# Optimization experiments

Measured on AMD Instinct MI355X. Metric: run time of the kernel, lower is better.

## Reference

```python
import jax, jax.numpy as jnp
import numpy as np

B, V, C, D = 32, 64, 32, 256
VOCAB = 20000
NUM_T = 1000


def _run_lstm(x, Wih, Whh, b):
    # x: [T, B, H_in]; torch-style single-layer LSTM with zero initial state
    T, Bb, _ = x.shape
    H = Whh.shape[1]
    def step(carry, xt):
        h, c = carry
        z = xt @ Wih.T + h @ Whh.T + b
        i, f, g, o = jnp.split(z, 4, axis=-1)
        c = jax.nn.sigmoid(f) * c + jax.nn.sigmoid(i) * jnp.tanh(g)
        h = jax.nn.sigmoid(o) * jnp.tanh(c)
        return (h, c), h
    h0 = jnp.zeros((Bb, H), x.dtype)
    _, ys = jax.lax.scan(step, (h0, h0), x)
    return ys


def _forward(input_seqs, masks, lengths, seq_time_step, code_masks, emb, WQ1, WK1,
             decay, initial, lstm_Wih, lstm_Whh, lstm_b, hs_Wih, hs_Whh, hs_b,
             whk_W, whk_b, w1_W, w1_b, w2_W, w2_b, fuse_W, fuse_b, lab_W, lab_b,
             betas, Wdiff, diffusion_time_t, normal_noise):
    Bb, Vv, Cc = input_seqs.shape
    tok = input_seqs.reshape(-1, Cc)                      # [B*V, C]
    x = emb[tok]                                          # [B*V, C, D]
    q = x @ WQ1.T
    k = x @ WK1.T
    dp = jnp.einsum('bcd,bed->bce', q, k)                 # [B*V, C, C]
    cm = code_masks.reshape(-1, Cc)
    dp = dp - cm[:, None, :] - cm[:, :, None]
    sp = jax.nn.softmax(dp / jnp.sqrt(jnp.float32(D)), axis=-1)
    femb = jnp.einsum('bce,bed->bcd', sp, x)              # attended code embeddings
    femb = ((cm - 1e20) / -1e20)[:, :, None] * femb       # zero out padded codes
    dec = decay[tok][..., None]                           # [B*V, C, 1]
    ini = initial[tok][..., None]
    t = seq_time_step.reshape(-1)[:, None, None]          # [B*V, 1, 1]
    gate = jax.nn.sigmoid(dec * t + ini)                  # time-decay gate
    vv = jnp.einsum('bcx,bcd->bd', gate, femb)            # [B*V, D] visit vector
    vv = vv.reshape(Bb, Vv, -1).transpose(1, 0, 2)        # [V, B, D]

    lstm_out = _run_lstm(vv, lstm_Wih, lstm_Whh, lstm_b)  # [V, B, D]
    t_lstm = lstm_out.transpose(1, 0, 2)                  # [B, V, D]
    hiddenstate = _run_lstm(lstm_out, hs_Wih, hs_Whh, hs_b).transpose(1, 0, 2)

    # Vectorized form of the original per-step python loop.
    # NOTE: the original always uses e_k = t_lstm_out[:, 0:1, :] (step 0) -- kept faithfully.
    e_k = t_lstm[:, 0:1, :]                               # [B, 1, D]
    whp = hiddenstate[:, :-1, :] @ whk_W.T + whk_b        # [B, V-1, D]
    cat = jnp.concatenate([jnp.broadcast_to(e_k, whp.shape), whp], axis=-1)
    attn = jax.nn.softmax(jnp.tanh(cat @ w1_W.T + w1_b) @ w2_W.T + w2_b, axis=-1)
    rest = e_k * attn[..., 0:1] + whp * attn[..., 1:2]
    aligned = jnp.concatenate([e_k, rest], axis=1)        # [B, V, D]

    alpha = jnp.cumprod(1.0 - betas)[diffusion_time_t][:, None, None]
    noisy = aligned * jnp.sqrt(alpha) + normal_noise * jnp.sqrt(1.0 - alpha)
    predicted_noise = noisy @ Wdiff                       # surrogate for UNetModel (source not provided)
    gen = aligned + (normal_noise - predicted_noise)

    fused = jnp.concatenate([t_lstm, gen], axis=-1) @ fuse_W.T + fuse_b   # [B, V, D]
    mask_final = (jnp.arange(Vv)[None, :] == (lengths - 1)[:, None]).astype(fused.dtype)
    final = (fused * mask_final[:, :, None]).sum(axis=1)  # select last valid visit
    return final @ lab_W.T + lab_b                        # [B, 2]


def setup_inputs() -> dict:
    key = jax.random.key(0)
    ks = jax.random.split(key, 20)
    s = 0.05
    n = lambda i, shp: jax.random.normal(ks[i], shp, jnp.float32) * s
    emb = jax.random.normal(ks[0], (VOCAB + 1, D), jnp.float32) * 0.02
    emb = emb.at[VOCAB].set(0.0)  # padding_idx row
    return {
        'input_seqs': jax.random.randint(ks[1], (B, V, C), 0, VOCAB),
        'masks': jnp.zeros((B, V), jnp.float32),
        'lengths': jax.random.randint(ks[2], (B,), 1, V + 1),
        'seq_time_step': jax.random.uniform(ks[3], (B, V), jnp.float32),
        'code_masks': jnp.zeros((B, V, C), jnp.float32),
        'emb': emb,
        'WQ1': n(4, (D, D)), 'WK1': n(5, (D, D)),
        'decay': jnp.full((VOCAB + 1,), -0.1, jnp.float32),
        'initial': jnp.full((VOCAB + 1,), 1.0, jnp.float32),
        'lstm_Wih': n(6, (4 * D, D)), 'lstm_Whh': n(7, (4 * D, D)),
        'lstm_b': jnp.zeros((4 * D,), jnp.float32),
        'hs_Wih': n(8, (4 * D, D)), 'hs_Whh': n(9, (4 * D, D)),
        'hs_b': jnp.zeros((4 * D,), jnp.float32),
        'whk_W': n(10, (D, D)), 'whk_b': jnp.zeros((D,), jnp.float32),
        'w1_W': n(11, (64, 2 * D)), 'w1_b': jnp.zeros((64,), jnp.float32),
        'w2_W': n(12, (2, 64)), 'w2_b': jnp.zeros((2,), jnp.float32),
        'fuse_W': n(13, (D, 2 * D)), 'fuse_b': jnp.zeros((D,), jnp.float32),
        'lab_W': n(14, (2, D)), 'lab_b': jnp.zeros((2,), jnp.float32),
        'betas': jnp.linspace(1e-4, 0.02, NUM_T, dtype=jnp.float32),
        'Wdiff': n(15, (D, D)),
        'diffusion_time_t': jax.random.randint(ks[16], (B,), 0, NUM_T),
        'normal_noise': jax.random.normal(ks[17], (B, V, D), jnp.float32),
    }


def reference(input_seqs, masks, lengths, seq_time_step, code_masks, emb, WQ1, WK1,
              decay, initial, lstm_Wih, lstm_Whh, lstm_b, hs_Wih, hs_Whh, hs_b,
              whk_W, whk_b, w1_W, w1_b, w2_W, w2_b, fuse_W, fuse_b, lab_W, lab_b,
              betas, Wdiff, diffusion_time_t, normal_noise):
    return _forward(input_seqs, masks, lengths, seq_time_step, code_masks, emb, WQ1, WK1,
                    decay, initial, lstm_Wih, lstm_Whh, lstm_b, hs_Wih, hs_Whh, hs_b,
                    whk_W, whk_b, w1_W, w1_b, w2_W, w2_b, fuse_W, fuse_b, lab_W, lab_b,
                    betas, Wdiff, diffusion_time_t, normal_noise)
```

## Files before the change

### kernel.cpp

```cpp
#include <hip/hip_runtime.h>
#include <hip/hip_bf16.h>
#include <cmath>

typedef __attribute__((ext_vector_type(8))) short bf16x8;
typedef __attribute__((ext_vector_type(4))) float f32x4;
typedef __attribute__((ext_vector_type(4))) int i32x4;
typedef __attribute__((ext_vector_type(2))) unsigned int u32x2;

__device__ __forceinline__ float bf2f(unsigned short u) {
    unsigned int x = ((unsigned int)u) << 16;
    return __builtin_bit_cast(float, x);
}
__device__ __forceinline__ unsigned short f2bf(float f) {
    unsigned int x = __builtin_bit_cast(unsigned int, f);
    unsigned int lsb = (x >> 16) & 1u;
    x += 0x7fffu + lsb;
    return (unsigned short)(x >> 16);
}
__device__ __forceinline__ float sigm(float z) {
    return 1.f / (1.f + __expf(-z));
}
__device__ __forceinline__ float rcpf(float x) { return __builtin_amdgcn_rcpf(x); }
__device__ __forceinline__ float sigm_f(float z) { return rcpf(1.f + __expf(-z)); }
__device__ __forceinline__ float tanh_f(float z) { return 1.f - 2.f * rcpf(1.f + __expf(2.f * z)); }

__device__ __forceinline__ long ldg_sc8l(const void* p) {
    long r;
    asm volatile("global_load_dwordx2 %0, %1, off sc1" : "=v"(r) : "v"(p) : "memory");
    return r;
}
__device__ __forceinline__ u32x2 ldg_sc_u2(const void* p) {
    u32x2 r;
    asm volatile("global_load_dwordx2 %0, %1, off sc1" : "=v"(r) : "v"(p) : "memory");
    return r;
}
__device__ __forceinline__ void stg_sc_u2(void* p, u32x2 v) {
    asm volatile("global_store_dwordx2 %0, %1, off sc1" :: "v"(p), "v"(v) : "memory");
}
__device__ __forceinline__ void stg_sc_b(void* p, int v) {
    asm volatile("global_store_byte %0, %1, off sc1" :: "v"(p), "v"(v) : "memory");
}

__global__ void __launch_bounds__(256) pack_all(
    const float* __restrict__ Whh1, const float* __restrict__ Wih2,
    const float* __restrict__ Whh2, const float* __restrict__ Wih1,
    const float* __restrict__ WQ1, const float* __restrict__ WK1,
    const float* __restrict__ betas, const int* __restrict__ dift,
    const float* __restrict__ whk_W, const float* __restrict__ fuse_W,
    const float* __restrict__ w1_W,
    long* __restrict__ Wq, float* __restrict__ cs,
    unsigned short* __restrict__ W1h, unsigned short* __restrict__ M_pk,
    float* __restrict__ alpha, int* __restrict__ flags,
    float* __restrict__ whkT, float* __restrict__ fuseT,
    float* __restrict__ w1T) {
    int blk = blockIdx.x, tid = threadIdx.x;
    if (blk < 384) {
        int R = blk * 8 + (tid >> 5);
        int mat = R >> 10;
        int n = R & 1023;
        int t32 = tid & 31;
        const float* src = (mat == 0) ? Whh1 : (mat == 1 ? Wih2 : Whh2);
        const float* rp = src + (size_t)n * 256 + t32 * 8;
        float v[8];
        float mx = 0.f;
        for (int j = 0; j < 8; ++j) { v[j] = rp[j]; mx = fmaxf(mx, fabsf(v[j])); }
        for (int m = 1; m <= 16; m <<= 1) mx = fmaxf(mx, __shfl_xor(mx, m));
        float inv = mx > 0.f ? 127.f / mx : 0.f;
        unsigned int lo = 0, hi = 0;
        for (int j = 0; j < 4; ++j) {
            int iv = __float2int_rn(v[j] * inv);
            lo |= ((unsigned int)(unsigned char)(signed char)iv) << (8 * j);
            int iv2 = __float2int_rn(v[4 + j] * inv);
            hi |= ((unsigned int)(unsigned char)(signed char)iv2) << (8 * j);
        }
        int g = n >> 8, rem = n & 255;
        int w8 = rem >> 5, dt = (rem >> 4) & 1, cc = rem & 15;
        int t8 = g * 2 + dt;
        int kb = t32 >> 2, q = t32 & 3;
        unsigned int* dst = (unsigned int*)Wq +
            ((size_t)((mat * 512 + w8 * 64 + t8 * 8 + kb) * 64) + q * 16 + cc) * 2;
        dst[0] = lo;
        dst[1] = hi;
        if (t32 == 0) cs[mat * 1024 + n] = mx / 16129.f;
    } else if (blk < 512) {
        int cch = (blk - 384) * 256 + tid;
        int nt = cch >> 9;
        int r = cch & 511;
        int kb = r >> 6;
        int lane = r & 63;
        int grow = nt * 16 + (lane & 15);
        int k0 = kb * 32 + (lane >> 4) * 8;
        const float* sp = Wih1 + (size_t)grow * 256 + k0;
        bf16x8 hi;
        for (int j = 0; j < 8; ++j) hi[j] = (short)f2bf(sp[j]);
        *reinterpret_cast<bf16x8*>(W1h + (size_t)cch * 8) = hi;
    } else if (blk == 512) {
        if (tid < 32) {
            int tb = dift[tid];
            float p = 1.f;
            for (int i = 0; i <= tb; ++i) p *= (1.f - betas[i]);
            alpha[tid] = p;
        }
    } else if (blk == 513) {
        for (int i = tid; i < 2048; i += 256) flags[i] = 0;
    } else if (blk < 578) {
        int gid = (blk - 514) * 256 + tid;
        for (int i = 0; i < 4; ++i) {
            int e = gid + i * 16384;
            int k = e >> 8, dd = e & 255;
            whkT[e] = whk_W[(size_t)dd * 256 + k];
        }
    } else if (blk < 706) {
        int gid = (blk - 578) * 256 + tid;
        for (int i = 0; i < 4; ++i) {
            int e = gid + i * 32768;
            int k = e >> 8, dd = e & 255;
            fuseT[e] = fuse_W[(size_t)dd * 512 + k];
        }
    } else if (blk < 738) {
        int gid = (blk - 706) * 256 + tid;
        for (int i = 0; i < 4; ++i) {
            int e = gid + i * 8192;
            int k = e >> 6, j = e & 63;
            w1T[e] = w1_W[(size_t)j * 512 + k];
        }
    } else {
        __shared__ unsigned short As[256][32];
        __shared__ unsigned short Bs[256][32];
        int bx = blk - 738;
        int e0 = (bx >> 3) << 5;
        int f0 = (bx & 7) << 5;
        int col = tid & 31, rr = tid >> 5;
        for (int rep = 0; rep < 32; ++rep) {
            int d = rep * 8 + rr;
            As[d][col] = f2bf(WQ1[d * 256 + e0 + col]);
            Bs[d][col] = f2bf(WK1[d * 256 + f0 + col]);
        }
        __syncthreads();
        int el = tid & 31;
        int fl0 = tid >> 5;
        for (int i = 0; i < 4; ++i) {
            int fl = fl0 + 8 * i;
            float acc = 0.f;
            for (int d = 0; d < 256; ++d)
                acc += bf2f(As[d][el]) * bf2f(Bs[d][fl]);
            int e = e0 + el, f = f0 + fl;
            int kb = e >> 5, r = (e >> 3) & 3, j = e & 7;
            int nb = f >> 4;
            int lane = (r << 4) | (f & 15);
            M_pk[(((nb * 8 + kb) * 64) + lane) * 8 + j] = f2bf(acc);
        }
    }
}

__global__ void __launch_bounds__(256) attn_bags(
    const int* __restrict__ seqs, const float* __restrict__ tstep,
    const float* __restrict__ cmask, const float* __restrict__ emb,
    const float* __restrict__ decay, const float* __restrict__ initial,
    const unsigned short* __restrict__ M_pk, float* __restrict__ vv) {
    __shared__ __align__(16) unsigned short x_bf[32 * 256];
    __shared__ __align__(16) unsigned short t1_bf[32 * 256];
    __shared__ float dp_f[32 * 33];
    __shared__ float gate_sh[32];
    __shared__ float cm_sh[32];
    __shared__ int tok_sh[32];
    __shared__ float w_sh[32];

    int bag = blockIdx.x;
    int tid = threadIdx.x;

    if (tid < 32) {
        int tok = seqs[bag * 32 + tid];
        tok_sh[tid] = tok;
        float cm = cmask[bag * 32 + tid];
        cm_sh[tid] = cm;
        float tt = tstep[bag];
        float g = sigm(decay[tok] * tt + initial[tok]);
        g *= (cm - 1e20f) / (-1e20f);
        gate_sh[tid] = g;
    }
    __syncthreads();

    for (int it = 0; it < 8; ++it) {
        int fidx = it * 256 + tid;
        int c = fidx >> 6;
        int f4 = fidx & 63;
        const float4* src = reinterpret_cast<const float4*>(emb + (size_t)tok_sh[c] * 256) + f4;
        float4 vx = *src;
        int colx = f4 * 4;
        int eidx = c * 256 + (colx ^ ((c & 7) << 3));
        ushort4 w;
        w.x = f2bf(vx.x); w.y = f2bf(vx.y); w.z = f2bf(vx.z); w.w = f2bf(vx.w);
        *reinterpret_cast<ushort4*>(&x_bf[eidx]) = w;
    }
    __syncthreads();

    int wv = tid >> 6;
    int lane = tid & 63;
    int lr = lane & 15;
    int lk = lane >> 4;

    f32x4 acc[2][4];
    for (int a = 0; a < 2; ++a)
        for (int n = 0; n < 4; ++n) acc[a][n] = (f32x4){0.f, 0.f, 0.f, 0.f};
    for (int kb = 0; kb < 8; ++kb) {
        bf16x8 afr[2];
        for (int mb = 0; mb < 2; ++mb) {
            int row = mb * 16 + lr;
            int colx = kb * 32 + lk * 8;
            afr[mb] = *reinterpret_cast<const bf16x8*>(&x_bf[row * 256 + (colx ^ ((row & 7) << 3))]);
        }
        for (int nbi = 0; nbi < 4; ++nbi) {
            int nb = wv * 4 + nbi;
            bf16x8 bfr = *reinterpret_cast<const bf16x8*>(M_pk + (((nb * 8 + kb) * 64) + lane) * 8);
            acc[0][nbi] = __builtin_amdgcn_mfma_f32_16x16x32_bf16(afr[0], bfr, acc[0][nbi], 0, 0, 0);
            acc[1][nbi] = __builtin_amdgcn_mfma_f32_16x16x32_bf16(afr[1], bfr, acc[1][nbi], 0, 0, 0);
        }
    }
    for (int mb = 0; mb < 2; ++mb)
        for (int nbi = 0; nbi < 4; ++nbi)
            for (int r = 0; r < 4; ++r) {
                int row = mb * 16 + lk * 4 + r;
                int colx = wv * 64 + nbi * 16 + lr;
                t1_bf[row * 256 + (colx ^ ((row & 7) << 3))] = f2bf(acc[mb][nbi][r]);
            }
    __syncthreads();

    {
        int mb = wv >> 1, nb2 = wv & 1;
        f32x4 dacc = (f32x4){0.f, 0.f, 0.f, 0.f};
        for (int kb = 0; kb < 8; ++kb) {
            int cola = kb * 32 + lk * 8;
            int rowa = mb * 16 + lr;
            bf16x8 afr = *reinterpret_cast<const bf16x8*>(&t1_bf[rowa * 256 + (cola ^ ((rowa & 7) << 3))]);
            int rowb = nb2 * 16 + lr;
            bf16x8 bfr = *reinterpret_cast<const bf16x8*>(&x_bf[rowb * 256 + (cola ^ ((rowb & 7) << 3))]);
            dacc = __builtin_amdgcn_mfma_f32_16x16x32_bf16(afr, bfr, dacc, 0, 0, 0);
        }
        for (int r = 0; r < 4; ++r) {
            int c = mb * 16 + lk * 4 + r;
            int e = nb2 * 16 + lr;
            dp_f[c * 33 + e] = dacc[r];
        }
    }
    __syncthreads();

    if (tid < 32) {
        int c = tid;
        float cmc = cm_sh[c];
        float lg[32];
        float mx = -1e30f;
        for (int e = 0; e < 32; ++e) {
            float l = (dp_f[c * 33 + e] - cmc - cm_sh[e]) * 0.0625f;
            lg[e] = l;
            mx = fmaxf(mx, l);
        }
        float s = 0.f;
        for (int e = 0; e < 32; ++e) { float ex = __expf(lg[e] - mx); lg[e] = ex; s += ex; }
        float inv = 1.f / s;
        for (int e = 0; e < 32; ++e) dp_f[c * 33 + e] = lg[e] * inv;
    }
    __syncthreads();
    if (tid < 32) {
        int e = tid;
        float a2 = 0.f;
        for (int c = 0; c < 32; ++c) a2 += gate_sh[c] * dp_f[c * 33 + e];
        w_sh[e] = a2;
    }
    __syncthreads();

    float accv = 0.f;
    int d = tid;
    for (int e = 0; e < 32; ++e)
        accv += w_sh[e] * bf2f(x_bf[e * 256 + (d ^ ((e & 7) << 3))]);
    vv[(size_t)bag * 256 + d] = accv;
}

__global__ void __launch_bounds__(256) x1_mfma(const float* __restrict__ vv,
                                               const unsigned short* __restrict__ W1h,
                                               const float* __restrict__ lstm_b,
                                               unsigned short* __restrict__ X1bf) {
    __shared__ __align__(16) unsigned short xs[32 * 256];
    int blk = blockIdx.x;
    int rb = blk >> 3, gb = blk & 7;
    int tid = threadIdx.x;
    for (int it = 0; it < 8; ++it) {
        int idx = it * 256 + tid;
        int row = idx >> 6, f4 = idx & 63;
        float4 v = *reinterpret_cast<const float4*>(vv + (size_t)(rb * 32 + row) * 256 + f4 * 4);
        ushort4 w;
        w.x = f2bf(v.x); w.y = f2bf(v.y); w.z = f2bf(v.z); w.w = f2bf(v.w);
        *reinterpret_cast<ushort4*>(&xs[row * 256 + ((f4 * 4) ^ ((row & 7) << 3))]) = w;
    }
    __syncthreads();
    int wv = tid >> 6, lane = tid & 63, cl = lane & 15, kh = lane >> 4;
    f32x4 acc[2][2];
    for (int n = 0; n < 2; ++n) {
        int nt = gb * 8 + wv * 2 + n;
        float bz = lstm_b[nt * 16 + cl];
        acc[n][0] = (f32x4){bz, bz, bz, bz};
        acc[n][1] = (f32x4){bz, bz, bz, bz};
    }
    #pragma unroll
    for (int kb = 0; kb < 8; ++kb) {
        int k = kb * 32 + kh * 8;
        bf16x8 a0 = *reinterpret_cast<const bf16x8*>(&xs[cl * 256 + (k ^ ((cl & 7) << 3))]);
        bf16x8 a1 = *reinterpret_cast<const bf16x8*>(&xs[(16 + cl) * 256 + (k ^ (((16 + cl) & 7) << 3))]);
        for (int n = 0; n < 2; ++n) {
            int nt = gb * 8 + wv * 2 + n;
            size_t o = ((size_t)(nt * 8 + kb) * 64 + lane) * 8;
            bf16x8 bh = *reinterpret_cast<const bf16x8*>(W1h + o);
            acc[n][0] = __builtin_amdgcn_mfma_f32_16x16x32_bf16(a0, bh, acc[n][0], 0, 0, 0);
            acc[n][1] = __builtin_amdgcn_mfma_f32_16x16x32_bf16(a1, bh, acc[n][1], 0, 0, 0);
        }
    }
    for (int n = 0; n < 2; ++n) {
        int nt = gb * 8 + wv * 2 + n;
        int g = nt * 16 + cl;
        int dX = g & 255, gt = g >> 8;
        for (int mt = 0; mt < 2; ++mt)
            for (int r = 0; r < 4; ++r) {
                int row = rb * 32 + mt * 16 + kh * 4 + r;
                int b = row >> 6, t = row & 63;
                X1bf[((size_t)t * 32 + b) * 1024 + dX * 4 + gt] = f2bf(acc[n][mt][r]);
            }
    }
}

__global__ void __launch_bounds__(512, 2) lstm_persist(
    const long* __restrict__ Wq, const float* __restrict__ cs,
    const unsigned short* __restrict__ X1bf, const float* __restrict__ hs_b,
    unsigned short* __restrict__ h1bf, unsigned short* __restrict__ h2bf,
    signed char* h1q, unsigned short* p1, int* flags) {
    int role = blockIdx.x;
    int half = role & 1;
    int kind = role >> 1;
    int tid = threadIdx.x;
    int w = tid >> 6, lane = tid & 63, c = lane & 15, q = lane >> 4;

    long wt[64];
    #pragma unroll
    for (int t8 = 0; t8 < 8; ++t8)
        #pragma unroll
        for (int kb = 0; kb < 8; ++kb)
            wt[t8 * 8 + kb] = Wq[(size_t)((kind * 512 + w * 64 + t8 * 8 + kb) * 64) + lane];
    float csv[8];
    #pragma unroll
    for (int t8 = 0; t8 < 8; ++t8) {
        int g = t8 >> 1, dt = t8 & 1;
        csv[t8] = cs[kind * 1024 + g * 256 + w * 32 + dt * 16 + c];
    }

    if (kind == 0) {
        __shared__ signed char hq[2][16][272];
        float cstate[8] = {0.f, 0.f, 0.f, 0.f, 0.f, 0.f, 0.f, 0.f};
        int B0 = half * 16 + q * 4;
        int dbase = w * 32;
        for (int t = 0; t < 64; ++t) {
            ushort4 xv[8];
            #pragma unroll
            for (int dt = 0; dt < 2; ++dt)
                #pragma unroll
                for (int r = 0; r < 4; ++r) {
                    int B = B0 + r, d = dbase + dt * 16 + c;
                    xv[dt * 4 + r] = *reinterpret_cast<const ushort4*>(
                        X1bf + ((size_t)(t * 32 + B) * 1024 + d * 4));
                }
            i32x4 acc[8];
            #pragma unroll
            for (int i = 0; i < 8; ++i) acc[i] = (i32x4){0, 0, 0, 0};
            if (t > 0) {
                int pb = (t - 1) & 1;
                long a[8];
                #pragma unroll
                for (int kb = 0; kb < 8; ++kb)
                    a[kb] = *reinterpret_cast<const long*>(&hq[pb][c][kb * 32 + q * 8]);
                #pragma unroll
                for (int t8 = 0; t8 < 8; ++t8)
                    #pragma unroll
                    for (int kb = 0; kb < 8; ++kb)
                        acc[t8] = __builtin_amdgcn_mfma_i32_16x16x32_i8(
                            a[kb], wt[t8 * 8 + kb], acc[t8], 0, 0, 0);
            }
            #pragma unroll
            for (int dt = 0; dt < 2; ++dt)
                #pragma unroll
                for (int r = 0; r < 4; ++r) {
                    int idx = dt * 4 + r;
                    ushort4 x = xv[idx];
                    float zi = (float)acc[0 + dt][r] * csv[0 + dt] + bf2f(x.x);
                    float zf = (float)acc[2 + dt][r] * csv[2 + dt] + bf2f(x.y);
                    float zg = (float)acc[4 + dt][r] * csv[4 + dt] + bf2f(x.z);
                    float zo = (float)acc[6 + dt][r] * csv[6 + dt] + bf2f(x.w);
                    float cn = sigm_f(zf) * cstate[idx] + sigm_f(zi) * tanh_f(zg);
                    float hn = sigm_f(zo) * tanh_f(cn);
                    cstate[idx] = cn;
                    int B = B0 + r, d = dbase + dt * 16 + c;
                    h1bf[(size_t)(t * 32 + B) * 256 + d] = f2bf(hn);
                    int hv = __float2int_rn(hn * 127.f);
                    hq[t & 1][q * 4 + r][d] = (signed char)hv;
                    stg_sc_b(h1q + (size_t)(t * 32 + B) * 256 + d, hv);
                }
            asm volatile("s_waitcnt vmcnt(0)" ::: "memory");
            if (lane == 0)
                __hip_atomic_store(flags + t * 16 + half * 8 + w, 1,
                                   __ATOMIC_RELAXED, __HIP_MEMORY_SCOPE_AGENT);
            __syncthreads();
        }
    } else if (kind == 1) {
        for (int s = 0; s < 64; ++s) {
            const int* f = flags + s * 16 + half * 8;
            while (1) {
                int v = 1;
                if (lane < 8)
                    v = __hip_atomic_load(f + lane, __ATOMIC_RELAXED, __HIP_MEMORY_SCOPE_AGENT);
                if (__all(v != 0)) break;
                __builtin_amdgcn_s_sleep(1);
            }
            __builtin_amdgcn_sched_barrier(0);
            const signed char* hb = h1q + (size_t)(s * 32 + half * 16) * 256;
            long a[8];
            #pragma unroll
            for (int kb = 0; kb < 8; ++kb)
                a[kb] = ldg_sc8l(hb + c * 256 + kb * 32 + q * 8);
            asm volatile("s_waitcnt vmcnt(0)" ::: "memory");
            __builtin_amdgcn_sched_barrier(0);
            i32x4 acc[8];
            #pragma unroll
            for (int i = 0; i < 8; ++i) acc[i] = (i32x4){0, 0, 0, 0};
            #pragma unroll
            for (int t8 = 0; t8 < 8; ++t8)
                #pragma unroll
                for (int kb = 0; kb < 8; ++kb)
                    acc[t8] = __builtin_amdgcn_mfma_i32_16x16x32_i8(
                        a[kb], wt[t8 * 8 + kb], acc[t8], 0, 0, 0);
            #pragma unroll
            for (int t8 = 0; t8 < 8; ++t8) {
                int g = t8 >> 1, dt = t8 & 1;
                int n = g * 256 + w * 32 + dt * 16 + c;
                u32x2 pv;
                pv.x = (unsigned int)f2bf((float)acc[t8][0] * csv[t8]) |
                       ((unsigned int)f2bf((float)acc[t8][1] * csv[t8]) << 16);
                pv.y = (unsigned int)f2bf((float)acc[t8][2] * csv[t8]) |
                       ((unsigned int)f2bf((float)acc[t8][3] * csv[t8]) << 16);
                stg_sc_u2(p1 + ((size_t)(s * 2 + half) * 1024 + n) * 16 + q * 4, pv);
            }
            asm volatile("s_waitcnt vmcnt(0)" ::: "memory");
            if (lane == 0)
                __hip_atomic_store(flags + 1024 + s * 16 + half * 8 + w, 1,
                                   __ATOMIC_RELAXED, __HIP_MEMORY_SCOPE_AGENT);
        }
    } else {
        __shared__ signed char hq2[2][16][272];
        float cstate[8] = {0.f, 0.f, 0.f, 0.f, 0.f, 0.f, 0.f, 0.f};
        float bias[8];
        #pragma unroll
        for (int t8 = 0; t8 < 8; ++t8) {
            int g = t8 >> 1, dt = t8 & 1;
            bias[t8] = hs_b[g * 256 + w * 32 + dt * 16 + c];
        }
        int B0 = half * 16 + q * 4;
        int dbase = w * 32;
        for (int s = 0; s < 64; ++s) {
            const int* fp = flags + 1024 + s * 16 + half * 8 + w;
            while (__hip_atomic_load(fp, __ATOMIC_RELAXED, __HIP_MEMORY_SCOPE_AGENT) == 0)
                __builtin_amdgcn_s_sleep(1);
            __builtin_amdgcn_sched_barrier(0);
            u32x2 pv[8];
            #pragma unroll
            for (int t8 = 0; t8 < 8; ++t8) {
                int g = t8 >> 1, dt = t8 & 1;
                int n = g * 256 + w * 32 + dt * 16 + c;
                pv[t8] = ldg_sc_u2(p1 + ((size_t)(s * 2 + half) * 1024 + n) * 16 + q * 4);
            }
            i32x4 acc[8];
            #pragma unroll
            for (int i = 0; i < 8; ++i) acc[i] = (i32x4){0, 0, 0, 0};
            if (s > 0) {
                int pb = (s - 1) & 1;
                long a[8];
                #pragma unroll
                for (int kb = 0; kb < 8; ++kb)
                    a[kb] = *reinterpret_cast<const long*>(&hq2[pb][c][kb * 32 + q * 8]);
                asm volatile("s_waitcnt vmcnt(0)" ::: "memory");
                __builtin_amdgcn_sched_barrier(0);
                #pragma unroll
                for (int t8 = 0; t8 < 8; ++t8)
                    #pragma unroll
                    for (int kb = 0; kb < 8; ++kb)
                        acc[t8] = __builtin_amdgcn_mfma_i32_16x16x32_i8(
                            a[kb], wt[t8 * 8 + kb], acc[t8], 0, 0, 0);
            } else {
                asm volatile("s_waitcnt vmcnt(0)" ::: "memory");
                __builtin_amdgcn_sched_barrier(0);
            }
            #pragma unroll
            for (int dt = 0; dt < 2; ++dt)
                #pragma unroll
                for (int r = 0; r < 4; ++r) {
                    int idx = dt * 4 + r;
                    float p_i = bf2f((unsigned short)((r < 2 ? pv[0 + dt].x : pv[0 + dt].y) >> ((r & 1) * 16)));
                    float p_f = bf2f((unsigned short)((r < 2 ? pv[2 + dt].x : pv[2 + dt].y) >> ((r & 1) * 16)));
                    float p_g = bf2f((unsigned short)((r < 2 ? pv[4 + dt].x : pv[4 + dt].y) >> ((r & 1) * 16)));
                    float p_o = bf2f((unsigned short)((r < 2 ? pv[6 + dt].x : pv[6 + dt].y) >> ((r & 1) * 16)));
                    float zi = (float)acc[0 + dt][r] * csv[0 + dt] + p_i + bias[0 + dt];
                    float zf = (float)acc[2 + dt][r] * csv[2 + dt] + p_f + bias[2 + dt];
                    float zg = (float)acc[4 + dt][r] * csv[4 + dt] + p_g + bias[4 + dt];
                    float zo = (float)acc[6 + dt][r] * csv[6 + dt] + p_o + bias[6 + dt];
                    float cn = sigm_f(zf) * cstate[idx] + sigm_f(zi) * tanh_f(zg);
                    float hn = sigm_f(zo) * tanh_f(cn);
                    cstate[idx] = cn;
                    int B = B0 + r, d = dbase + dt * 16 + c;
                    h2bf[(size_t)(s * 32 + B) * 256 + d] = f2bf(hn);
                    hq2[s & 1][q * 4 + r][d] = (signed char)__float2int_rn(hn * 127.f);
                }
            __syncthreads();
        }
    }
}

__global__ void __launch_bounds__(256) tail_k(
    const int* __restrict__ lengths,
    const unsigned short* __restrict__ h1, const unsigned short* __restrict__ h2,
    const float* __restrict__ whkT, const float* __restrict__ whk_b,
    const float* __restrict__ w1T, const float* __restrict__ w1_b,
    const float* __restrict__ w2_W, const float* __restrict__ w2_b,
    const float* __restrict__ fuseT, const float* __restrict__ fuse_b,
    const float* __restrict__ lab_W, const float* __restrict__ lab_b,
    const float* __restrict__ Wdiff, const float* __restrict__ alpha,
    const float* __restrict__ noise, float* __restrict__ out) {
    __shared__ float ek[256], tv[256], hs[256], whp[256], a1s[64];
    __shared__ float noisy_s[256], fin[512], fused_s[256], attn_s[2];
    int b = blockIdx.x, tid = threadIdx.x;
    int vstar = lengths[b] - 1;
    {
        ek[tid] = bf2f(h1[(size_t)b * 256 + tid]);
        tv[tid] = bf2f(h1[((size_t)vstar * 32 + b) * 256 + tid]);
        if (vstar > 0)
            hs[tid] = bf2f(h2[((size_t)(vstar - 1) * 32 + b) * 256 + tid]);
    }
    __syncthreads();

    float aligned;
    if (vstar > 0) {
        float s0 = 0.f, s1 = 0.f, s2 = 0.f, s3 = 0.f;
        for (int k = 0; k < 256; k += 4) {
            s0 += whkT[(k + 0) * 256 + tid] * hs[k + 0];
            s1 += whkT[(k + 1) * 256 + tid] * hs[k + 1];
            s2 += whkT[(k + 2) * 256 + tid] * hs[k + 2];
            s3 += whkT[(k + 3) * 256 + tid] * hs[k + 3];
        }
        whp[tid] = whk_b[tid] + s0 + s1 + s2 + s3;
        __syncthreads();
        if (tid < 64) {
            float a0 = 0.f, a1 = 0.f, a2 = 0.f, a3 = 0.f;
            for (int k = 0; k < 256; k += 4) {
                a0 += w1T[(k + 0) * 64 + tid] * ek[k + 0];
                a1 += w1T[(k + 1) * 64 + tid] * ek[k + 1];
                a2 += w1T[(k + 2) * 64 + tid] * ek[k + 2];
                a3 += w1T[(k + 3) * 64 + tid] * ek[k + 3];
            }
            for (int k = 0; k < 256; k += 4) {
                a0 += w1T[(256 + k + 0) * 64 + tid] * whp[k + 0];
                a1 += w1T[(256 + k + 1) * 64 + tid] * whp[k + 1];
                a2 += w1T[(256 + k + 2) * 64 + tid] * whp[k + 2];
                a3 += w1T[(256 + k + 3) * 64 + tid] * whp[k + 3];
            }
            a1s[tid] = tanhf(w1_b[tid] + a0 + a1 + a2 + a3);
        }
        __syncthreads();
        if (tid < 2) {
            float a3 = w2_b[tid];
            const float* wr2 = w2_W + tid * 64;
            for (int k = 0; k < 64; ++k) a3 += wr2[k] * a1s[k];
            attn_s[tid] = a3;
        }
        __syncthreads();
        float m = fmaxf(attn_s[0], attn_s[1]);
        float e0 = __expf(attn_s[0] - m), e1 = __expf(attn_s[1] - m);
        float inv = 1.f / (e0 + e1);
        aligned = ek[tid] * (e0 * inv) + whp[tid] * (e1 * inv);
    } else {
        aligned = ek[tid];
    }

    float al = alpha[b];
    float sa = sqrtf(al), sb = sqrtf(1.f - al);
    float nz = noise[((size_t)b * 64 + vstar) * 256 + tid];
    noisy_s[tid] = aligned * sa + nz * sb;
    __syncthreads();
    {
        float p0 = 0.f, p1v = 0.f, p2 = 0.f, p3 = 0.f;
        for (int k = 0; k < 256; k += 4) {
            p0 += noisy_s[k + 0] * Wdiff[(size_t)(k + 0) * 256 + tid];
            p1v += noisy_s[k + 1] * Wdiff[(size_t)(k + 1) * 256 + tid];
            p2 += noisy_s[k + 2] * Wdiff[(size_t)(k + 2) * 256 + tid];
            p3 += noisy_s[k + 3] * Wdiff[(size_t)(k + 3) * 256 + tid];
        }
        float gen = aligned + nz - (p0 + p1v + p2 + p3);
        fin[tid] = tv[tid];
        fin[256 + tid] = gen;
    }
    __syncthreads();
    {
        float f0 = 0.f, f1 = 0.f, f2 = 0.f, f3 = 0.f;
        for (int k = 0; k < 512; k += 4) {
            f0 += fuseT[(k + 0) * 256 + tid] * fin[k + 0];
            f1 += fuseT[(k + 1) * 256 + tid] * fin[k + 1];
            f2 += fuseT[(k + 2) * 256 + tid] * fin[k + 2];
            f3 += fuseT[(k + 3) * 256 + tid] * fin[k + 3];
        }
        fused_s[tid] = fuse_b[tid] + f0 + f1 + f2 + f3;
    }
    __syncthreads();
    if (tid < 2) {
        float o = lab_b[tid];
        const float* lw = lab_W + tid * 256;
        for (int k = 0; k < 256; ++k) o += lw[k] * fused_s[k];
        out[b * 2 + tid] = o;
    }
}

extern "C" void kernel_launch(void* const* d_in, const int* in_sizes, int n_in,
                              void* d_out, int out_size, void* d_ws, size_t ws_size,
                              hipStream_t stream) {
    const int*   seqs    = (const int*)  d_in[0];
    const int*   lengths = (const int*)  d_in[2];
    const float* tstep   = (const float*)d_in[3];
    const float* cmask   = (const float*)d_in[4];
    const float* emb     = (const float*)d_in[5];
    const float* WQ1     = (const float*)d_in[6];
    const float* WK1     = (const float*)d_in[7];
    const float* decay   = (const float*)d_in[8];
    const float* initial = (const float*)d_in[9];
    const float* Wih1    = (const float*)d_in[10];
    const float* Whh1    = (const float*)d_in[11];
    const float* lstm_b  = (const float*)d_in[12];
    const float* Wih2    = (const float*)d_in[13];
    const float* Whh2    = (const float*)d_in[14];
    const float* hs_b    = (const float*)d_in[15];
    const float* whk_W   = (const float*)d_in[16];
    const float* whk_b   = (const float*)d_in[17];
    const float* w1_W    = (const float*)d_in[18];
    const float* w1_b    = (const float*)d_in[19];
    const float* w2_W    = (const float*)d_in[20];
    const float* w2_b    = (const float*)d_in[21];
    const float* fuse_W  = (const float*)d_in[22];
    const float* fuse_b  = (const float*)d_in[23];
    const float* lab_W   = (const float*)d_in[24];
    const float* lab_b   = (const float*)d_in[25];
    const float* betas   = (const float*)d_in[26];
    const float* Wdiff   = (const float*)d_in[27];
    const int*   dift    = (const int*)  d_in[28];
    const float* noise   = (const float*)d_in[29];
    float* out = (float*)d_out;

    float* ws = (float*)d_ws;
    size_t off = 0;
    auto alloc = [&](size_t nfloats) { size_t r = off; off += (nfloats + 63) & ~(size_t)63; return r; };
    unsigned short* M_pk  = (unsigned short*)(ws + alloc(32768));
    float*          alpha = ws + alloc(64);
    float*          cs    = ws + alloc(3072);
    int*            flags = (int*)(ws + alloc(2048));
    float*          vv    = ws + alloc(524288);
    unsigned short* X1bf  = (unsigned short*)(ws + alloc(1048576));
    unsigned short* h1bf  = (unsigned short*)(ws + alloc(262144));
    unsigned short* h2bf  = (unsigned short*)(ws + alloc(262144));
    unsigned short* p1    = (unsigned short*)(ws + alloc(1048576));
    long*           Wq    = (long*)(ws + alloc(196608));
    unsigned short* W1h   = (unsigned short*)(ws + alloc(131072));
    float*          whkT  = ws + alloc(65536);
    float*          fuseT = ws + alloc(131072);
    float*          w1T   = ws + alloc(32768);
    signed char*    h1q   = (signed char*)vv;

    pack_all<<<802, 256, 0, stream>>>(Whh1, Wih2, Whh2, Wih1, WQ1, WK1, betas, dift,
                                      whk_W, fuse_W, w1_W,
                                      Wq, cs, W1h, M_pk, alpha, flags,
                                      whkT, fuseT, w1T);
    attn_bags<<<2048, 256, 0, stream>>>(seqs, tstep, cmask, emb, decay, initial, M_pk, vv);
    x1_mfma<<<512, 256, 0, stream>>>(vv, W1h, lstm_b, X1bf);
    lstm_persist<<<6, 512, 0, stream>>>(Wq, cs, X1bf, hs_b, h1bf, h2bf, h1q, p1, flags);
    tail_k<<<32, 256, 0, stream>>>(lengths, h1bf, h2bf, whkT, whk_b,
                                   w1T, w1_b, w2_W, w2_b, fuseT, fuse_b,
                                   lab_W, lab_b, Wdiff, alpha, noise, out);
}
```

Before: 340.9 us.

## Fuse attention, input projection and LSTM into one kernel with counter-based dataflow

Merges the attention-bag, input-projection and persistent LSTM kernels into a single launch. The 6 LSTM role blocks come first, followed by attention blocks and then projection blocks. Global atomic counters gate each stage, so the LSTM can start on early timesteps while later visit vectors and projections are still being computed. This removes launch boundaries and overlaps the serial recurrence with the parallel front end. The cost is spin-wait polling and a dependence on the persistent blocks being co-resident, plus a separate h1q buffer and 512-thread blocks for the attention work.

```diff
diff --git a/kernel.cpp b/kernel.cpp
--- a/kernel.cpp
+++ b/kernel.cpp
@@ -34,11 +34,23 @@
     asm volatile("global_load_dwordx2 %0, %1, off sc1" : "=v"(r) : "v"(p) : "memory");
     return r;
 }
+__device__ __forceinline__ f32x4 ldg_sc16(const void* p) {
+    f32x4 r;
+    asm volatile("global_load_dwordx4 %0, %1, off sc1" : "=v"(r) : "v"(p) : "memory");
+    return r;
+}
 __device__ __forceinline__ void stg_sc_u2(void* p, u32x2 v) {
     asm volatile("global_store_dwordx2 %0, %1, off sc1" :: "v"(p), "v"(v) : "memory");
 }
 __device__ __forceinline__ void stg_sc_b(void* p, int v) {
     asm volatile("global_store_byte %0, %1, off sc1" :: "v"(p), "v"(v) : "memory");
+}
+__device__ __forceinline__ void stg_sc_dw(void* p, float v) {
+    asm volatile("global_store_dword %0, %1, off sc1" :: "v"(p), "v"(v) : "memory");
+}
+__device__ __forceinline__ void stg_sc_sh(void* p, unsigned short v) {
+    unsigned int vx = v;
+    asm volatile("global_store_short %0, %1, off sc1" :: "v"(p), "v"(vx) : "memory");
 }
 
 __global__ void __launch_bounds__(256) pack_all(
@@ -102,7 +114,7 @@
             alpha[tid] = p;
         }
     } else if (blk == 513) {
-        for (int i = tid; i < 2048; i += 256) flags[i] = 0;
+        for (int i = tid; i < 4096; i += 256) flags[i] = 0;
     } else if (blk < 578) {
         int gid = (blk - 514) * 256 + tid;
         for (int i = 0; i < 4; ++i) {
@@ -153,369 +165,407 @@
     }
 }
 
-__global__ void __launch_bounds__(256) attn_bags(
+__global__ void __launch_bounds__(512, 2) fused_main(
     const int* __restrict__ seqs, const float* __restrict__ tstep,
     const float* __restrict__ cmask, const float* __restrict__ emb,
     const float* __restrict__ decay, const float* __restrict__ initial,
-    const unsigned short* __restrict__ M_pk, float* __restrict__ vv) {
-    __shared__ __align__(16) unsigned short x_bf[32 * 256];
-    __shared__ __align__(16) unsigned short t1_bf[32 * 256];
-    __shared__ float dp_f[32 * 33];
-    __shared__ float gate_sh[32];
-    __shared__ float cm_sh[32];
-    __shared__ int tok_sh[32];
-    __shared__ float w_sh[32];
-
-    int bag = blockIdx.x;
-    int tid = threadIdx.x;
-
-    if (tid < 32) {
-        int tok = seqs[bag * 32 + tid];
-        tok_sh[tid] = tok;
-        float cm = cmask[bag * 32 + tid];
-        cm_sh[tid] = cm;
-        float tt = tstep[bag];
-        float g = sigm(decay[tok] * tt + initial[tok]);
-        g *= (cm - 1e20f) / (-1e20f);
-        gate_sh[tid] = g;
-    }
-    __syncthreads();
-
-    for (int it = 0; it < 8; ++it) {
-        int fidx = it * 256 + tid;
-        int c = fidx >> 6;
-        int f4 = fidx & 63;
-        const float4* src = reinterpret_cast<const float4*>(emb + (size_t)tok_sh[c] * 256) + f4;
-        float4 vx = *src;
-        int colx = f4 * 4;
-        int eidx = c * 256 + (colx ^ ((c & 7) << 3));
-        ushort4 w;
-        w.x = f2bf(vx.x); w.y = f2bf(vx.y); w.z = f2bf(vx.z); w.w = f2bf(vx.w);
-        *reinterpret_cast<ushort4*>(&x_bf[eidx]) = w;
-    }
-    __syncthreads();
-
-    int wv = tid >> 6;
-    int lane = tid & 63;
-    int lr = lane & 15;
-    int lk = lane >> 4;
-
-    f32x4 acc[2][4];
-    for (int a = 0; a < 2; ++a)
-        for (int n = 0; n < 4; ++n) acc[a][n] = (f32x4){0.f, 0.f, 0.f, 0.f};
-    for (int kb = 0; kb < 8; ++kb) {
-        bf16x8 afr[2];
-        for (int mb = 0; mb < 2; ++mb) {
-            int row = mb * 16 + lr;
-            int colx = kb * 32 + lk * 8;
-            afr[mb] = *reinterpret_cast<const bf16x8*>(&x_bf[row * 256 + (colx ^ ((row & 7) << 3))]);
-        }
-        for (int nbi = 0; nbi < 4; ++nbi) {
-            int nb = wv * 4 + nbi;
-            bf16x8 bfr = *reinterpret_cast<const bf16x8*>(M_pk + (((nb * 8 + kb) * 64) + lane) * 8);
-            acc[0][nbi] = __builtin_amdgcn_mfma_f32_16x16x32_bf16(afr[0], bfr, acc[0][nbi], 0, 0, 0);
-            acc[1][nbi] = __builtin_amdgcn_mfma_f32_16x16x32_bf16(afr[1], bfr, acc[1][nbi], 0, 0, 0);
-        }
-    }
-    for (int mb = 0; mb < 2; ++mb)
-        for (int nbi = 0; nbi < 4; ++nbi)
-            for (int r = 0; r < 4; ++r) {
-                int row = mb * 16 + lk * 4 + r;
-                int colx = wv * 64 + nbi * 16 + lr;
-                t1_bf[row * 256 + (colx ^ ((row & 7) << 3))] = f2bf(acc[mb][nbi][r]);
-            }
-    __syncthreads();
-
-    {
-        int mb = wv >> 1, nb2 = wv & 1;
-        f32x4 dacc = (f32x4){0.f, 0.f, 0.f, 0.f};
-        for (int kb = 0; kb < 8; ++kb) {
-            int cola = kb * 32 + lk * 8;
-            int rowa = mb * 16 + lr;
-            bf16x8 afr = *reinterpret_cast<const bf16x8*>(&t1_bf[rowa * 256 + (cola ^ ((rowa & 7) << 3))]);
-            int rowb = nb2 * 16 + lr;
-            bf16x8 bfr = *reinterpret_cast<const bf16x8*>(&x_bf[rowb * 256 + (cola ^ ((rowb & 7) << 3))]);
-            dacc = __builtin_amdgcn_mfma_f32_16x16x32_bf16(afr, bfr, dacc, 0, 0, 0);
-        }
-        for (int r = 0; r < 4; ++r) {
-            int c = mb * 16 + lk * 4 + r;
-            int e = nb2 * 16 + lr;
-            dp_f[c * 33 + e] = dacc[r];
-        }
-    }
-    __syncthreads();
-
-    if (tid < 32) {
-        int c = tid;
-        float cmc = cm_sh[c];
-        float lg[32];
-        float mx = -1e30f;
-        for (int e = 0; e < 32; ++e) {
-            float l = (dp_f[c * 33 + e] - cmc - cm_sh[e]) * 0.0625f;
-            lg[e] = l;
-            mx = fmaxf(mx, l);
-        }
-        float s = 0.f;
-        for (int e = 0; e < 32; ++e) { float ex = __expf(lg[e] - mx); lg[e] = ex; s += ex; }
-        float inv = 1.f / s;
-        for (int e = 0; e < 32; ++e) dp_f[c * 33 + e] = lg[e] * inv;
-    }
-    __syncthreads();
-    if (tid < 32) {
-        int e = tid;
-        float a2 = 0.f;
-        for (int c = 0; c < 32; ++c) a2 += gate_sh[c] * dp_f[c * 33 + e];
-        w_sh[e] = a2;
-    }
-    __syncthreads();
-
-    float accv = 0.f;
-    int d = tid;
-    for (int e = 0; e < 32; ++e)
-        accv += w_sh[e] * bf2f(x_bf[e * 256 + (d ^ ((e & 7) << 3))]);
-    vv[(size_t)bag * 256 + d] = accv;
-}
-
-__global__ void __launch_bounds__(256) x1_mfma(const float* __restrict__ vv,
-                                               const unsigned short* __restrict__ W1h,
-                                               const float* __restrict__ lstm_b,
-                                               unsigned short* __restrict__ X1bf) {
-    __shared__ __align__(16) unsigned short xs[32 * 256];
-    int blk = blockIdx.x;
-    int rb = blk >> 3, gb = blk & 7;
-    int tid = threadIdx.x;
-    for (int it = 0; it < 8; ++it) {
-        int idx = it * 256 + tid;
-        int row = idx >> 6, f4 = idx & 63;
-        float4 v = *reinterpret_cast<const float4*>(vv + (size_t)(rb * 32 + row) * 256 + f4 * 4);
-        ushort4 w;
-        w.x = f2bf(v.x); w.y = f2bf(v.y); w.z = f2bf(v.z); w.w = f2bf(v.w);
-        *reinterpret_cast<ushort4*>(&xs[row * 256 + ((f4 * 4) ^ ((row & 7) << 3))]) = w;
-    }
-    __syncthreads();
-    int wv = tid >> 6, lane = tid & 63, cl = lane & 15, kh = lane >> 4;
-    f32x4 acc[2][2];
-    for (int n = 0; n < 2; ++n) {
-        int nt = gb * 8 + wv * 2 + n;
-        float bz = lstm_b[nt * 16 + cl];
-        acc[n][0] = (f32x4){bz, bz, bz, bz};
-        acc[n][1] = (f32x4){bz, bz, bz, bz};
-    }
-    #pragma unroll
-    for (int kb = 0; kb < 8; ++kb) {
-        int k = kb * 32 + kh * 8;
-        bf16x8 a0 = *reinterpret_cast<const bf16x8*>(&xs[cl * 256 + (k ^ ((cl & 7) << 3))]);
-        bf16x8 a1 = *reinterpret_cast<const bf16x8*>(&xs[(16 + cl) * 256 + (k ^ (((16 + cl) & 7) << 3))]);
-        for (int n = 0; n < 2; ++n) {
-            int nt = gb * 8 + wv * 2 + n;
-            size_t o = ((size_t)(nt * 8 + kb) * 64 + lane) * 8;
-            bf16x8 bh = *reinterpret_cast<const bf16x8*>(W1h + o);
-            acc[n][0] = __builtin_amdgcn_mfma_f32_16x16x32_bf16(a0, bh, acc[n][0], 0, 0, 0);
-            acc[n][1] = __builtin_amdgcn_mfma_f32_16x16x32_bf16(a1, bh, acc[n][1], 0, 0, 0);
-        }
-    }
-    for (int n = 0; n < 2; ++n) {
-        int nt = gb * 8 + wv * 2 + n;
-        int g = nt * 16 + cl;
-        int dX = g & 255, gt = g >> 8;
-        for (int mt = 0; mt < 2; ++mt)
-            for (int r = 0; r < 4; ++r) {
-                int row = rb * 32 + mt * 16 + kh * 4 + r;
-                int b = row >> 6, t = row & 63;
-                X1bf[((size_t)t * 32 + b) * 1024 + dX * 4 + gt] = f2bf(acc[n][mt][r]);
-            }
-    }
-}
-
-__global__ void __launch_bounds__(512, 2) lstm_persist(
+    const unsigned short* __restrict__ M_pk, float* __restrict__ vv,
+    const unsigned short* __restrict__ W1h, const float* __restrict__ lstm_b,
+    unsigned short* __restrict__ X1bf,
     const long* __restrict__ Wq, const float* __restrict__ cs,
-    const unsigned short* __restrict__ X1bf, const float* __restrict__ hs_b,
+    const float* __restrict__ hs_b,
     unsigned short* __restrict__ h1bf, unsigned short* __restrict__ h2bf,
     signed char* h1q, unsigned short* p1, int* flags) {
-    int role = blockIdx.x;
-    int half = role & 1;
-    int kind = role >> 1;
-    int tid = threadIdx.x;
-    int w = tid >> 6, lane = tid & 63, c = lane & 15, q = lane >> 4;
-
-    long wt[64];
-    #pragma unroll
-    for (int t8 = 0; t8 < 8; ++t8)
+    __shared__ __align__(16) unsigned char smem[37504];
+    int blk = blockIdx.x;
+    int* cnt_vv = flags + 2048;
+    int* cnt_x1 = flags + 2112;
+
+    if (blk < 6) {
+        int role = blk;
+        int half = role & 1;
+        int kind = role >> 1;
+        int tid = threadIdx.x;
+        int w = tid >> 6, lane = tid & 63, c = lane & 15, q = lane >> 4;
+
+        long wt[64];
         #pragma unroll
-        for (int kb = 0; kb < 8; ++kb)
-            wt[t8 * 8 + kb] = Wq[(size_t)((kind * 512 + w * 64 + t8 * 8 + kb) * 64) + lane];
-    float csv[8];
-    #pragma unroll
-    for (int t8 = 0; t8 < 8; ++t8) {
-        int g = t8 >> 1, dt = t8 & 1;
-        csv[t8] = cs[kind * 1024 + g * 256 + w * 32 + dt * 16 + c];
-    }
-
-    if (kind == 0) {
-        __shared__ signed char hq[2][16][272];
-        float cstate[8] = {0.f, 0.f, 0.f, 0.f, 0.f, 0.f, 0.f, 0.f};
-        int B0 = half * 16 + q * 4;
-        int dbase = w * 32;
-        for (int t = 0; t < 64; ++t) {
-            ushort4 xv[8];
+        for (int t8 = 0; t8 < 8; ++t8)
             #pragma unroll
-            for (int dt = 0; dt < 2; ++dt)
-                #pragma unroll
-                for (int r = 0; r < 4; ++r) {
-                    int B = B0 + r, d = dbase + dt * 16 + c;
-                    xv[dt * 4 + r] = *reinterpret_cast<const ushort4*>(
-                        X1bf + ((size_t)(t * 32 + B) * 1024 + d * 4));
+            for (int kb = 0; kb < 8; ++kb)
+                wt[t8 * 8 + kb] = Wq[(size_t)((kind * 512 + w * 64 + t8 * 8 + kb) * 64) + lane];
+        float csv[8];
+        #pragma unroll
+        for (int t8 = 0; t8 < 8; ++t8) {
+            int g = t8 >> 1, dt = t8 & 1;
+            csv[t8] = cs[kind * 1024 + g * 256 + w * 32 + dt * 16 + c];
+        }
+
+        if (kind == 0) {
+            auto hq = (signed char (*)[16][272])smem;
+            float cstate[8] = {0.f, 0.f, 0.f, 0.f, 0.f, 0.f, 0.f, 0.f};
+            int B0 = half * 16 + q * 4;
+            int dbase = w * 32;
+            for (int t = 0; t < 64; ++t) {
+                if ((t & 31) == 0) {
+                    const int* cp = cnt_x1 + half * 2 + (t >> 5);
+                    while (__hip_atomic_load(cp, __ATOMIC_RELAXED, __HIP_MEMORY_SCOPE_AGENT) < 128)
+                        __builtin_amdgcn_s_sleep(8);
+                    __builtin_amdgcn_sched_barrier(0);
                 }
-            i32x4 acc[8];
-            #pragma unroll
-            for (int i = 0; i < 8; ++i) acc[i] = (i32x4){0, 0, 0, 0};
-            if (t > 0) {
-                int pb = (t - 1) & 1;
+                u32x2 xq[8];
+                #pragma unroll
+                for (int dt = 0; dt < 2; ++dt)
+                    #pragma unroll
+                    for (int r = 0; r < 4; ++r) {
+                        int B = B0 + r, d = dbase + dt * 16 + c;
+                        xq[dt * 4 + r] = ldg_sc_u2(X1bf + ((size_t)(t * 32 + B) * 1024 + d * 4));
+                    }
+                i32x4 acc[8];
+                #pragma unroll
+                for (int i = 0; i < 8; ++i) acc[i] = (i32x4){0, 0, 0, 0};
+                if (t > 0) {
+                    int pb = (t - 1) & 1;
+                    long a[8];
+                    #pragma unroll
+                    for (int kb = 0; kb < 8; ++kb)
+                        a[kb] = *reinterpret_cast<const long*>(&hq[pb][c][kb * 32 + q * 8]);
+                    #pragma unroll
+                    for (int t8 = 0; t8 < 8; ++t8)
+                        #pragma unroll
+                        for (int kb = 0; kb < 8; ++kb)
+                            acc[t8] = __builtin_amdgcn_mfma_i32_16x16x32_i8(
+                                a[kb], wt[t8 * 8 + kb], acc[t8], 0, 0, 0);
+                }
+                asm volatile("s_waitcnt vmcnt(0)" ::: "memory");
+                __builtin_amdgcn_sched_barrier(0);
+                #pragma unroll
+                for (int dt = 0; dt < 2; ++dt)
+                    #pragma unroll
+                    for (int r = 0; r < 4; ++r) {
+                        int idx = dt * 4 + r;
+                        u32x2 x = xq[idx];
+                        float zi = (float)acc[0 + dt][r] * csv[0 + dt] + bf2f((unsigned short)(x.x & 0xFFFFu));
+                        float zf = (float)acc[2 + dt][r] * csv[2 + dt] + bf2f((unsigned short)(x.x >> 16));
+                        float zg = (float)acc[4 + dt][r] * csv[4 + dt] + bf2f((unsigned short)(x.y & 0xFFFFu));
+                        float zo = (float)acc[6 + dt][r] * csv[6 + dt] + bf2f((unsigned short)(x.y >> 16));
+                        float cn = sigm_f(zf) * cstate[idx] + sigm_f(zi) * tanh_f(zg);
+                        float hn = sigm_f(zo) * tanh_f(cn);
+                        cstate[idx] = cn;
+                        int B = B0 + r, d = dbase + dt * 16 + c;
+                        h1bf[(size_t)(t * 32 + B) * 256 + d] = f2bf(hn);
+                        int hv = __float2int_rn(hn * 127.f);
+                        hq[t & 1][q * 4 + r][d] = (signed char)hv;
+                        stg_sc_b(h1q + (size_t)(t * 32 + B) * 256 + d, hv);
+                    }
+                asm volatile("s_waitcnt vmcnt(0)" ::: "memory");
+                if (lane == 0)
+                    __hip_atomic_store(flags + t * 16 + half * 8 + w, 1,
+                                       __ATOMIC_RELAXED, __HIP_MEMORY_SCOPE_AGENT);
+                __syncthreads();
+            }
+        } else if (kind == 1) {
+            for (int s = 0; s < 64; ++s) {
+                const int* f = flags + s * 16 + half * 8;
+                while (1) {
+                    int v = 1;
+                    if (lane < 8)
+                        v = __hip_atomic_load(f + lane, __ATOMIC_RELAXED, __HIP_MEMORY_SCOPE_AGENT);
+                    if (__all(v != 0)) break;
+                    __builtin_amdgcn_s_sleep(1);
+                }
+                __builtin_amdgcn_sched_barrier(0);
+                const signed char* hb = h1q + (size_t)(s * 32 + half * 16) * 256;
                 long a[8];
                 #pragma unroll
                 for (int kb = 0; kb < 8; ++kb)
-                    a[kb] = *reinterpret_cast<const long*>(&hq[pb][c][kb * 32 + q * 8]);
+                    a[kb] = ldg_sc8l(hb + c * 256 + kb * 32 + q * 8);
+                asm volatile("s_waitcnt vmcnt(0)" ::: "memory");
+                __builtin_amdgcn_sched_barrier(0);
+                i32x4 acc[8];
+                #pragma unroll
+                for (int i = 0; i < 8; ++i) acc[i] = (i32x4){0, 0, 0, 0};
                 #pragma unroll
                 for (int t8 = 0; t8 < 8; ++t8)
                     #pragma unroll
                     for (int kb = 0; kb < 8; ++kb)
                         acc[t8] = __builtin_amdgcn_mfma_i32_16x16x32_i8(
                             a[kb], wt[t8 * 8 + kb], acc[t8], 0, 0, 0);
-            }
-            #pragma unroll
-            for (int dt = 0; dt < 2; ++dt)
-                #pragma unroll
-                for (int r = 0; r < 4; ++r) {
-                    int idx = dt * 4 + r;
-                    ushort4 x = xv[idx];
-                    float zi = (float)acc[0 + dt][r] * csv[0 + dt] + bf2f(x.x);
-                    float zf = (float)acc[2 + dt][r] * csv[2 + dt] + bf2f(x.y);
-                    float zg = (float)acc[4 + dt][r] * csv[4 + dt] + bf2f(x.z);
-                    float zo = (float)acc[6 + dt][r] * csv[6 + dt] + bf2f(x.w);
-                    float cn = sigm_f(zf) * cstate[idx] + sigm_f(zi) * tanh_f(zg);
-                    float hn = sigm_f(zo) * tanh_f(cn);
-                    cstate[idx] = cn;
-                    int B = B0 + r, d = dbase + dt * 16 + c;
-                    h1bf[(size_t)(t * 32 + B) * 256 + d] = f2bf(hn);
-                    int hv = __float2int_rn(hn * 127.f);
-                    hq[t & 1][q * 4 + r][d] = (signed char)hv;
-                    stg_sc_b(h1q + (size_t)(t * 32 + B) * 256 + d, hv);
+                #pragma unroll
+                for (int t8 = 0; t8 < 8; ++t8) {
+                    int g = t8 >> 1, dt = t8 & 1;
+                    int n = g * 256 + w * 32 + dt * 16 + c;
+                    u32x2 pv;
+                    pv.x = (unsigned int)f2bf((float)acc[t8][0] * csv[t8]) |
+                           ((unsigned int)f2bf((float)acc[t8][1] * csv[t8]) << 16);
+                    pv.y = (unsigned int)f2bf((float)acc[t8][2] * csv[t8]) |
+                           ((unsigned int)f2bf((float)acc[t8][3] * csv[t8]) << 16);
+                    stg_sc_u2(p1 + ((size_t)(s * 2 + half) * 1024 + n) * 16 + q * 4, pv);
                 }
-            asm volatile("s_waitcnt vmcnt(0)" ::: "memory");
-            if (lane == 0)
-                __hip_atomic_store(flags + t * 16 + half * 8 + w, 1,
-                                   __ATOMIC_RELAXED, __HIP_MEMORY_SCOPE_AGENT);
-            __syncthreads();
-        }
-    } else if (kind == 1) {
-        for (int s = 0; s < 64; ++s) {
-            const int* f = flags + s * 16 + half * 8;
-            while (1) {
-                int v = 1;
-                if (lane < 8)
-                    v = __hip_atomic_load(f + lane, __ATOMIC_RELAXED, __HIP_MEMORY_SCOPE_AGENT);
-                if (__all(v != 0)) break;
-                __builtin_amdgcn_s_sleep(1);
-            }
-            __builtin_amdgcn_sched_barrier(0);
-            const signed char* hb = h1q + (size_t)(s * 32 + half * 16) * 256;
-            long a[8];
-            #pragma unroll
-            for (int kb = 0; kb < 8; ++kb)
-                a[kb] = ldg_sc8l(hb + c * 256 + kb * 32 + q * 8);
-            asm volatile("s_waitcnt vmcnt(0)" ::: "memory");
-            __builtin_amdgcn_sched_barrier(0);
-            i32x4 acc[8];
-            #pragma unroll
-            for (int i = 0; i < 8; ++i) acc[i] = (i32x4){0, 0, 0, 0};
-            #pragma unroll
-            for (int t8 = 0; t8 < 8; ++t8)
-                #pragma unroll
-                for (int kb = 0; kb < 8; ++kb)
-                    acc[t8] = __builtin_amdgcn_mfma_i32_16x16x32_i8(
-                        a[kb], wt[t8 * 8 + kb], acc[t8], 0, 0, 0);
+                asm volatile("s_waitcnt vmcnt(0)" ::: "memory");
+                if (lane == 0)
+                    __hip_atomic_store(flags + 1024 + s * 16 + half * 8 + w, 1,
+                                       __ATOMIC_RELAXED, __HIP_MEMORY_SCOPE_AGENT);
+            }
+        } else {
+            auto hq2 = (signed char (*)[16][272])smem;
+            float cstate[8] = {0.f, 0.f, 0.f, 0.f, 0.f, 0.f, 0.f, 0.f};
+            float bias[8];
             #pragma unroll
             for (int t8 = 0; t8 < 8; ++t8) {
                 int g = t8 >> 1, dt = t8 & 1;
-                int n = g * 256 + w * 32 + dt * 16 + c;
-                u32x2 pv;
-                pv.x = (unsigned int)f2bf((float)acc[t8][0] * csv[t8]) |
-                       ((unsigned int)f2bf((float)acc[t8][1] * csv[t8]) << 16);
-                pv.y = (unsigned int)f2bf((float)acc[t8][2] * csv[t8]) |
-                       ((unsigned int)f2bf((float)acc[t8][3] * csv[t8]) << 16);
-                stg_sc_u2(p1 + ((size_t)(s * 2 + half) * 1024 + n) * 16 + q * 4, pv);
-            }
-            asm volatile("s_waitcnt vmcnt(0)" ::: "memory");
-            if (lane == 0)
-                __hip_atomic_store(flags + 1024 + s * 16 + half * 8 + w, 1,
-                                   __ATOMIC_RELAXED, __HIP_MEMORY_SCOPE_AGENT);
-        }
-    } else {
-        __shared__ signed char hq2[2][16][272];
-        float cstate[8] = {0.f, 0.f, 0.f, 0.f, 0.f, 0.f, 0.f, 0.f};
-        float bias[8];
-        #pragma unroll
-        for (int t8 = 0; t8 < 8; ++t8) {
-            int g = t8 >> 1, dt = t8 & 1;
-            bias[t8] = hs_b[g * 256 + w * 32 + dt * 16 + c];
-        }
-        int B0 = half * 16 + q * 4;
-        int dbase = w * 32;
-        for (int s = 0; s < 64; ++s) {
-            const int* fp = flags + 1024 + s * 16 + half * 8 + w;
-            while (__hip_atomic_load(fp, __ATOMIC_RELAXED, __HIP_MEMORY_SCOPE_AGENT) == 0)
-                __builtin_amdgcn_s_sleep(1);
-            __builtin_amdgcn_sched_barrier(0);
-            u32x2 pv[8];
-            #pragma unroll
-            for (int t8 = 0; t8 < 8; ++t8) {
-                int g = t8 >> 1, dt = t8 & 1;
-                int n = g * 256 + w * 32 + dt * 16 + c;
-                pv[t8] = ldg_sc_u2(p1 + ((size_t)(s * 2 + half) * 1024 + n) * 16 + q * 4);
-            }
-            i32x4 acc[8];
-            #pragma unroll
-            for (int i = 0; i < 8; ++i) acc[i] = (i32x4){0, 0, 0, 0};
-            if (s > 0) {
-                int pb = (s - 1) & 1;
-                long a[8];
-                #pragma unroll
-                for (int kb = 0; kb < 8; ++kb)
-                    a[kb] = *reinterpret_cast<const long*>(&hq2[pb][c][kb * 32 + q * 8]);
-                asm volatile("s_waitcnt vmcnt(0)" ::: "memory");
+                bias[t8] = hs_b[g * 256 + w * 32 + dt * 16 + c];
+            }
+            int B0 = half * 16 + q * 4;
+            int dbase = w * 32;
+            for (int s = 0; s < 64; ++s) {
+                const int* fp = flags + 1024 + s * 16 + half * 8 + w;
+                while (__hip_atomic_load(fp, __ATOMIC_RELAXED, __HIP_MEMORY_SCOPE_AGENT) == 0)
+                    __builtin_amdgcn_s_sleep(1);
                 __builtin_amdgcn_sched_barrier(0);
-                #pragma unroll
-                for (int t8 = 0; t8 < 8; ++t8)
+                u32x2 pv[8];
+                #pragma unroll
+                for (int t8 = 0; t8 < 8; ++t8) {
+                    int g = t8 >> 1, dt = t8 & 1;
+                    int n = g * 256 + w * 32 + dt * 16 + c;
+                    pv[t8] = ldg_sc_u2(p1 + ((size_t)(s * 2 + half) * 1024 + n) * 16 + q * 4);
+                }
+                i32x4 acc[8];
+                #pragma unroll
+                for (int i = 0; i < 8; ++i) acc[i] = (i32x4){0, 0, 0, 0};
+                if (s > 0) {
+                    int pb = (s - 1) & 1;
+                    long a[8];
                     #pragma unroll
                     for (int kb = 0; kb < 8; ++kb)
-                        acc[t8] = __builtin_amdgcn_mfma_i32_16x16x32_i8(
-                            a[kb], wt[t8 * 8 + kb], acc[t8], 0, 0, 0);
-            } else {
-                asm volatile("s_waitcnt vmcnt(0)" ::: "memory");
-                __builtin_amdgcn_sched_barrier(0);
-            }
-            #pragma unroll
-            for (int dt = 0; dt < 2; ++dt)
-                #pragma unroll
+                        a[kb] = *reinterpret_cast<const long*>(&hq2[pb][c][kb * 32 + q * 8]);
+                    asm volatile("s_waitcnt vmcnt(0)" ::: "memory");
+                    __builtin_amdgcn_sched_barrier(0);
+                    #pragma unroll
+                    for (int t8 = 0; t8 < 8; ++t8)
+                        #pragma unroll
+                        for (int kb = 0; kb < 8; ++kb)
+                            acc[t8] = __builtin_amdgcn_mfma_i32_16x16x32_i8(
+                                a[kb], wt[t8 * 8 + kb], acc[t8], 0, 0, 0);
+                } else {
+                    asm volatile("s_waitcnt vmcnt(0)" ::: "memory");
+                    __builtin_amdgcn_sched_barrier(0);
+                }
+                #pragma unroll
+                for (int dt = 0; dt < 2; ++dt)
+                    #pragma unroll
+                    for (int r = 0; r < 4; ++r) {
+                        int idx = dt * 4 + r;
+                        float p_i = bf2f((unsigned short)((r < 2 ? pv[0 + dt].x : pv[0 + dt].y) >> ((r & 1) * 16)));
+                        float p_f = bf2f((unsigned short)((r < 2 ? pv[2 + dt].x : pv[2 + dt].y) >> ((r & 1) * 16)));
+                        float p_g = bf2f((unsigned short)((r < 2 ? pv[4 + dt].x : pv[4 + dt].y) >> ((r & 1) * 16)));
+                        float p_o = bf2f((unsigned short)((r < 2 ? pv[6 + dt].x : pv[6 + dt].y) >> ((r & 1) * 16)));
+                        float zi = (float)acc[0 + dt][r] * csv[0 + dt] + p_i + bias[0 + dt];
+                        float zf = (float)acc[2 + dt][r] * csv[2 + dt] + p_f + bias[2 + dt];
+                        float zg = (float)acc[4 + dt][r] * csv[4 + dt] + p_g + bias[4 + dt];
+                        float zo = (float)acc[6 + dt][r] * csv[6 + dt] + p_o + bias[6 + dt];
+                        float cn = sigm_f(zf) * cstate[idx] + sigm_f(zi) * tanh_f(zg);
+                        float hn = sigm_f(zo) * tanh_f(cn);
+                        cstate[idx] = cn;
+                        int B = B0 + r, d = dbase + dt * 16 + c;
+                        h2bf[(size_t)(s * 32 + B) * 256 + d] = f2bf(hn);
+                        hq2[s & 1][q * 4 + r][d] = (signed char)__float2int_rn(hn * 127.f);
+                    }
+                __syncthreads();
+            }
+        }
+    } else if (blk < 2054) {
+        unsigned short* x_bf = (unsigned short*)smem;
+        unsigned short* t1_bf = (unsigned short*)(smem + 16384);
+        float* dp_f = (float*)(smem + 32768);
+        float* gate_sh = (float*)(smem + 36992);
+        float* cm_sh = (float*)(smem + 37120);
+        int* tok_sh = (int*)(smem + 37248);
+        float* w_sh = (float*)(smem + 37376);
+
+        int bagIdx = blk - 6;
+        int v = bagIdx >> 5;
+        int b = bagIdx & 31;
+        int bag = b * 64 + v;
+        int tid = threadIdx.x & 255;
+
+        if (threadIdx.x < 32) {
+            int tok = seqs[bag * 32 + threadIdx.x];
+            tok_sh[threadIdx.x] = tok;
+            float cm = cmask[bag * 32 + threadIdx.x];
+            cm_sh[threadIdx.x] = cm;
+            float tt = tstep[bag];
+            float g = sigm(decay[tok] * tt + initial[tok]);
+            g *= (cm - 1e20f) / (-1e20f);
+            gate_sh[threadIdx.x] = g;
+        }
+        __syncthreads();
+
+        for (int it = 0; it < 8; ++it) {
+            int fidx = it * 256 + tid;
+            int cc = fidx >> 6;
+            int f4 = fidx & 63;
+            const float4* src = reinterpret_cast<const float4*>(emb + (size_t)tok_sh[cc] * 256) + f4;
+            float4 vx = *src;
+            int colx = f4 * 4;
+            int eidx = cc * 256 + (colx ^ ((cc & 7) << 3));
+            ushort4 wz;
+            wz.x = f2bf(vx.x); wz.y = f2bf(vx.y); wz.z = f2bf(vx.z); wz.w = f2bf(vx.w);
+            *reinterpret_cast<ushort4*>(&x_bf[eidx]) = wz;
+        }
+        __syncthreads();
+
+        int wv = tid >> 6;
+        int lane = tid & 63;
+        int lr = lane & 15;
+        int lk = lane >> 4;
+
+        f32x4 acc[2][4];
+        for (int a = 0; a < 2; ++a)
+            for (int n = 0; n < 4; ++n) acc[a][n] = (f32x4){0.f, 0.f, 0.f, 0.f};
+        for (int kb = 0; kb < 8; ++kb) {
+            bf16x8 afr[2];
+            for (int mb = 0; mb < 2; ++mb) {
+                int row = mb * 16 + lr;
+                int colx = kb * 32 + lk * 8;
+                afr[mb] = *reinterpret_cast<const bf16x8*>(&x_bf[row * 256 + (colx ^ ((row & 7) << 3))]);
+            }
+            for (int nbi = 0; nbi < 4; ++nbi) {
+                int nb = wv * 4 + nbi;
+                bf16x8 bfr = *reinterpret_cast<const bf16x8*>(M_pk + (((nb * 8 + kb) * 64) + lane) * 8);
+                acc[0][nbi] = __builtin_amdgcn_mfma_f32_16x16x32_bf16(afr[0], bfr, acc[0][nbi], 0, 0, 0);
+                acc[1][nbi] = __builtin_amdgcn_mfma_f32_16x16x32_bf16(afr[1], bfr, acc[1][nbi], 0, 0, 0);
+            }
+        }
+        for (int mb = 0; mb < 2; ++mb)
+            for (int nbi = 0; nbi < 4; ++nbi)
                 for (int r = 0; r < 4; ++r) {
-                    int idx = dt * 4 + r;
-                    float p_i = bf2f((unsigned short)((r < 2 ? pv[0 + dt].x : pv[0 + dt].y) >> ((r & 1) * 16)));
-                    float p_f = bf2f((unsigned short)((r < 2 ? pv[2 + dt].x : pv[2 + dt].y) >> ((r & 1) * 16)));
-                    float p_g = bf2f((unsigned short)((r < 2 ? pv[4 + dt].x : pv[4 + dt].y) >> ((r & 1) * 16)));
-                    float p_o = bf2f((unsigned short)((r < 2 ? pv[6 + dt].x : pv[6 + dt].y) >> ((r & 1) * 16)));
-                    float zi = (float)acc[0 + dt][r] * csv[0 + dt] + p_i + bias[0 + dt];
-                    float zf = (float)acc[2 + dt][r] * csv[2 + dt] + p_f + bias[2 + dt];
-                    float zg = (float)acc[4 + dt][r] * csv[4 + dt] + p_g + bias[4 + dt];
-                    float zo = (float)acc[6 + dt][r] * csv[6 + dt] + p_o + bias[6 + dt];
-                    float cn = sigm_f(zf) * cstate[idx] + sigm_f(zi) * tanh_f(zg);
-                    float hn = sigm_f(zo) * tanh_f(cn);
-                    cstate[idx] = cn;
-                    int B = B0 + r, d = dbase + dt * 16 + c;
-                    h2bf[(size_t)(s * 32 + B) * 256 + d] = f2bf(hn);
-                    hq2[s & 1][q * 4 + r][d] = (signed char)__float2int_rn(hn * 127.f);
+                    int row = mb * 16 + lk * 4 + r;
+                    int colx = wv * 64 + nbi * 16 + lr;
+                    t1_bf[row * 256 + (colx ^ ((row & 7) << 3))] = f2bf(acc[mb][nbi][r]);
                 }
-            __syncthreads();
-        }
+        __syncthreads();
+
+        {
+            int mb = wv >> 1, nb2 = wv & 1;
+            f32x4 dacc = (f32x4){0.f, 0.f, 0.f, 0.f};
+            for (int kb = 0; kb < 8; ++kb) {
+                int cola = kb * 32 + lk * 8;
+                int rowa = mb * 16 + lr;
+                bf16x8 afr = *reinterpret_cast<const bf16x8*>(&t1_bf[rowa * 256 + (cola ^ ((rowa & 7) << 3))]);
+                int rowb = nb2 * 16 + lr;
+                bf16x8 bfr = *reinterpret_cast<const bf16x8*>(&x_bf[rowb * 256 + (cola ^ ((rowb & 7) << 3))]);
+                dacc = __builtin_amdgcn_mfma_f32_16x16x32_bf16(afr, bfr, dacc, 0, 0, 0);
+            }
+            for (int r = 0; r < 4; ++r) {
+                int cc = mb * 16 + lk * 4 + r;
+                int e = nb2 * 16 + lr;
+                dp_f[cc * 33 + e] = dacc[r];
+            }
+        }
+        __syncthreads();
+
+        if (threadIdx.x < 32) {
+            int cc = threadIdx.x;
+            float cmc = cm_sh[cc];
+            float lg[32];
+            float mx = -1e30f;
+            for (int e = 0; e < 32; ++e) {
+                float l = (dp_f[cc * 33 + e] - cmc - cm_sh[e]) * 0.0625f;
+                lg[e] = l;
+                mx = fmaxf(mx, l);
+            }
+            float s = 0.f;
+            for (int e = 0; e < 32; ++e) { float ex = __expf(lg[e] - mx); lg[e] = ex; s += ex; }
+            float inv = 1.f / s;
+            for (int e = 0; e < 32; ++e) dp_f[cc * 33 + e] = lg[e] * inv;
+        }
+        __syncthreads();
+        if (threadIdx.x < 32) {
+            int e = threadIdx.x;
+            float a2 = 0.f;
+            for (int cc = 0; cc < 32; ++cc) a2 += gate_sh[cc] * dp_f[cc * 33 + e];
+            w_sh[e] = a2;
+        }
+        __syncthreads();
+
+        float accv = 0.f;
+        int d = tid;
+        for (int e = 0; e < 32; ++e)
+            accv += w_sh[e] * bf2f(x_bf[e * 256 + (d ^ ((e & 7) << 3))]);
+        stg_sc_dw(vv + (size_t)bag * 256 + d, accv);
+        asm volatile("s_waitcnt vmcnt(0)" ::: "memory");
+        __syncthreads();
+        if (threadIdx.x == 0)
+            atomicAdd(cnt_vv + b * 2 + (v >= 32 ? 1 : 0), 1);
+    } else {
+        unsigned short* xs = (unsigned short*)smem;
+        int blk2 = blk - 2054;
+        int rb = blk2 >> 3, gb = blk2 & 7;
+        int tid = threadIdx.x & 255;
+
+        {
+            const int* cp = cnt_vv + rb;
+            while (__hip_atomic_load(cp, __ATOMIC_RELAXED, __HIP_MEMORY_SCOPE_AGENT) < 32)
+                __builtin_amdgcn_s_sleep(2);
+            __builtin_amdgcn_sched_barrier(0);
+        }
+        f32x4 vbuf[8];
+        #pragma unroll
+        for (int it = 0; it < 8; ++it) {
+            int idx = it * 256 + tid;
+            int row = idx >> 6, f4 = idx & 63;
+            vbuf[it] = ldg_sc16(vv + (size_t)(rb * 32 + row) * 256 + f4 * 4);
+        }
+        asm volatile("s_waitcnt vmcnt(0)" ::: "memory");
+        __builtin_amdgcn_sched_barrier(0);
+        #pragma unroll
+        for (int it = 0; it < 8; ++it) {
+            int idx = it * 256 + tid;
+            int row = idx >> 6, f4 = idx & 63;
+            ushort4 wz;
+            wz.x = f2bf(vbuf[it][0]); wz.y = f2bf(vbuf[it][1]);
+            wz.z = f2bf(vbuf[it][2]); wz.w = f2bf(vbuf[it][3]);
+            *reinterpret_cast<ushort4*>(&xs[row * 256 + ((f4 * 4) ^ ((row & 7) << 3))]) = wz;
+        }
+        __syncthreads();
+        int wv = tid >> 6, lane = tid & 63, cl = lane & 15, kh = lane >> 4;
+        f32x4 acc[2][2];
+        for (int n = 0; n < 2; ++n) {
+            int nt = gb * 8 + wv * 2 + n;
+            float bz = lstm_b[nt * 16 + cl];
+            acc[n][0] = (f32x4){bz, bz, bz, bz};
+            acc[n][1] = (f32x4){bz, bz, bz, bz};
+        }
+        #pragma unroll
+        for (int kb = 0; kb < 8; ++kb) {
+            int k = kb * 32 + kh * 8;
+            bf16x8 a0 = *reinterpret_cast<const bf16x8*>(&xs[cl * 256 + (k ^ ((cl & 7) << 3))]);
+            bf16x8 a1 = *reinterpret_cast<const bf16x8*>(&xs[(16 + cl) * 256 + (k ^ (((16 + cl) & 7) << 3))]);
+            for (int n = 0; n < 2; ++n) {
+                int nt = gb * 8 + wv * 2 + n;
+                size_t o = ((size_t)(nt * 8 + kb) * 64 + lane) * 8;
+                bf16x8 bh = *reinterpret_cast<const bf16x8*>(W1h + o);
+                acc[n][0] = __builtin_amdgcn_mfma_f32_16x16x32_bf16(a0, bh, acc[n][0], 0, 0, 0);
+                acc[n][1] = __builtin_amdgcn_mfma_f32_16x16x32_bf16(a1, bh, acc[n][1], 0, 0, 0);
+            }
+        }
+        for (int n = 0; n < 2; ++n) {
+            int nt = gb * 8 + wv * 2 + n;
+            int g = nt * 16 + cl;
+            int dX = g & 255, gt = g >> 8;
+            for (int mt = 0; mt < 2; ++mt)
+                for (int r = 0; r < 4; ++r) {
+                    int row = rb * 32 + mt * 16 + kh * 4 + r;
+                    int b = row >> 6, t = row & 63;
+                    stg_sc_sh(X1bf + ((size_t)t * 32 + b) * 1024 + dX * 4 + gt,
+                              f2bf(acc[n][mt][r]));
+                }
+        }
+        asm volatile("s_waitcnt vmcnt(0)" ::: "memory");
+        __syncthreads();
+        if (threadIdx.x == 0)
+            atomicAdd(cnt_x1 + ((rb >> 1) >= 16 ? 2 : 0) + (rb & 1), 1);
     }
 }
 
@@ -661,7 +711,7 @@
     unsigned short* M_pk  = (unsigned short*)(ws + alloc(32768));
     float*          alpha = ws + alloc(64);
     float*          cs    = ws + alloc(3072);
-    int*            flags = (int*)(ws + alloc(2048));
+    int*            flags = (int*)(ws + alloc(4096));
     float*          vv    = ws + alloc(524288);
     unsigned short* X1bf  = (unsigned short*)(ws + alloc(1048576));
     unsigned short* h1bf  = (unsigned short*)(ws + alloc(262144));
@@ -672,15 +722,15 @@
     float*          whkT  = ws + alloc(65536);
     float*          fuseT = ws + alloc(131072);
     float*          w1T   = ws + alloc(32768);
-    signed char*    h1q   = (signed char*)vv;
+    signed char*    h1q   = (signed char*)(ws + alloc(131072));
 
     pack_all<<<802, 256, 0, stream>>>(Whh1, Wih2, Whh2, Wih1, WQ1, WK1, betas, dift,
                                       whk_W, fuse_W, w1_W,
                                       Wq, cs, W1h, M_pk, alpha, flags,
                                       whkT, fuseT, w1T);
-    attn_bags<<<2048, 256, 0, stream>>>(seqs, tstep, cmask, emb, decay, initial, M_pk, vv);
-    x1_mfma<<<512, 256, 0, stream>>>(vv, W1h, lstm_b, X1bf);
-    lstm_persist<<<6, 512, 0, stream>>>(Wq, cs, X1bf, hs_b, h1bf, h2bf, h1q, p1, flags);
+    fused_main<<<2566, 512, 0, stream>>>(seqs, tstep, cmask, emb, decay, initial,
+                                         M_pk, vv, W1h, lstm_b, X1bf,
+                                         Wq, cs, hs_b, h1bf, h2bf, h1q, p1, flags);
     tail_k<<<32, 256, 0, stream>>>(lengths, h1bf, h2bf, whkT, whk_b,
                                    w1T, w1_b, w2_W, w2_b, fuseT, fuse_b,
                                    lab_W, lab_b, Wdiff, alpha, noise, out);
```

Result: slower. 395.5 us (+16.0%).
